# Kernel optimization log

Measured on AMD Instinct MI355X. Metric: run time of the kernel, lower is better.

## Reference

```python
import jax, jax.numpy as jnp
import numpy as np

B, T, E, H, DK, FF = 8, 2048, 64, 8, 8, 256
EPS = 1e-5


def _ln(x, g, b):
    m = jnp.mean(x, axis=-1, keepdims=True)
    v = jnp.mean((x - m) ** 2, axis=-1, keepdims=True)
    return (x - m) * jax.lax.rsqrt(v + EPS) * g + b


def setup_inputs() -> dict:
    key = jax.random.key(0)
    ks = jax.random.split(key, 16)
    s = 0.05
    f32 = jnp.float32
    return {
        "x": jax.random.normal(ks[0], (B, T, E), f32),
        "Wq": jax.random.normal(ks[1], (E, E), f32) * s,
        "bq": jnp.zeros((E,), f32),
        "Wk": jax.random.normal(ks[2], (E, E), f32) * s,
        "bk": jnp.zeros((E,), f32),
        "Wv": jax.random.normal(ks[3], (E, E), f32) * s,
        "bv": jnp.zeros((E,), f32),
        "Wo": jax.random.normal(ks[4], (E, E), f32) * s,
        "bo": jnp.zeros((E,), f32),
        "theta_attn": jax.random.uniform(ks[5], (), f32, 0.0, 2.0 * np.pi),
        "theta_ffn": jax.random.uniform(ks[6], (), f32, 0.0, 2.0 * np.pi),
        "W1": jax.random.normal(ks[7], (FF, E), f32) * s,
        "b1": jnp.zeros((FF,), f32),
        "W2": jax.random.normal(ks[8], (E, FF), f32) * s,
        "b2": jnp.zeros((E,), f32),
        "g1": jnp.ones((E,), f32),
        "be1": jnp.zeros((E,), f32),
        "g2": jnp.ones((E,), f32),
        "be2": jnp.zeros((E,), f32),
    }


def _forward(x, Wq, bq, Wk, bk, Wv, bv, Wo, bo, theta_attn, theta_ffn,
             W1, b1, W2, b2, g1, be1, g2, be2):
    def split(h):  # [B,T,E] -> [B,H,T,DK]
        return h.reshape(B, T, H, DK).transpose(0, 2, 1, 3)

    q = split(x @ Wq.T + bq)
    k = split(x @ Wk.T + bk)
    v = split(x @ Wv.T + bv)
    # per-head quantum circuit: RX(x) then shared RX(theta) -> <Z> = cos(x + theta)
    q = jnp.cos(q + theta_attn)
    k = jnp.cos(k + theta_attn)
    v = jnp.cos(v + theta_attn)
    scores = jnp.einsum('bhtd,bhsd->bhts', q, k) / np.float32(np.sqrt(DK))
    scores = jax.nn.softmax(scores, axis=-1)
    attn = jnp.einsum('bhts,bhsd->bhtd', scores, v)
    attn = attn.transpose(0, 2, 1, 3).reshape(B, T, E) @ Wo.T + bo
    x1 = _ln(x + attn, g1, be1)
    # FFN quantum circuit: RX(x) then shared RY(theta) -> <Z> = cos(x)*cos(theta)
    qout = jnp.cos(x1) * jnp.cos(theta_ffn)
    f = jax.nn.relu(qout @ W1.T + b1) @ W2.T + b2
    return _ln(x1 + f, g2, be2)


def reference(x, Wq, bq, Wk, bk, Wv, bv, Wo, bo, theta_attn, theta_ffn,
              W1, b1, W2, b2, g1, be1, g2, be2):
    return _forward(x, Wq, bq, Wk, bk, Wv, bv, Wo, bo, theta_attn, theta_ffn,
                    W1, b1, W2, b2, g1, be1, g2, be2)
```

## Files before the change

kernel.cpp:

```cpp
#include <hip/hip_runtime.h>
#include <hip/hip_bf16.h>

#define B_ 8
#define T_ 2048
#define NROWS 16384

typedef __attribute__((ext_vector_type(4))) float f32x4;
typedef __attribute__((ext_vector_type(16))) float f32x16;
typedef __attribute__((ext_vector_type(8))) short short8;
typedef __fp16 half2_t __attribute__((ext_vector_type(2)));

__device__ __forceinline__ unsigned short f2bf(float f) {
    __hip_bfloat16 h = __float2bfloat16(f);
    return *reinterpret_cast<unsigned short*>(&h);
}
__device__ __forceinline__ unsigned int pkrtz(float a, float b) {
    half2_t h = __builtin_amdgcn_cvt_pkrtz(a, b);
    return __builtin_bit_cast(unsigned int, h);
}
__device__ __forceinline__ float dot2(unsigned int a, unsigned int b, float c) {
    return __builtin_amdgcn_fdot2(__builtin_bit_cast(half2_t, a),
                                  __builtin_bit_cast(half2_t, b), c, false);
}
__device__ __forceinline__ float fast_exp2(float x) {
#if __has_builtin(__builtin_amdgcn_exp2f)
    return __builtin_amdgcn_exp2f(x);
#else
    return exp2f(x);
#endif
}

__global__ __launch_bounds__(512, 4) void qkv_kernel(
    const float* __restrict__ x,
    const float* __restrict__ Wq, const float* __restrict__ bq,
    const float* __restrict__ Wk, const float* __restrict__ bk,
    const float* __restrict__ Wv, const float* __restrict__ bv,
    const float* __restrict__ theta_attn,
    unsigned short* __restrict__ qb, unsigned short* __restrict__ kbuf,
    unsigned short* __restrict__ vbuf)
{
    __shared__ unsigned int xpk[32][34];
    __shared__ unsigned int wpk[32][196];
    __shared__ unsigned short outs[32][216];
    const int tid = threadIdx.x;
    const int n0 = blockIdx.x * 32;

    {
        float4 v = ((const float4*)(x + (size_t)n0 * 64))[tid];
        int r = tid >> 4, k0 = (tid & 15) * 4;
        xpk[(k0 >> 1) + 0][r] = pkrtz(v.x, v.y);
        xpk[(k0 >> 1) + 1][r] = pkrtz(v.z, v.w);
    }
    const float* Wm[3] = {Wq, Wk, Wv};
    #pragma unroll
    for (int t = 0; t < 6; t++) {
        int fi = tid + t * 512;
        int m = fi >> 10, j = (fi >> 4) & 63, k0 = (fi & 15) * 4;
        float4 v = ((const float4*)Wm[m])[fi & 1023];
        wpk[(k0 >> 1) + 0][m * 64 + j] = pkrtz(v.x, v.y);
        wpk[(k0 >> 1) + 1][m * 64 + j] = pkrtz(v.z, v.w);
    }
    __syncthreads();

    const int r = tid >> 4;
    const int c0 = (tid & 15) * 12;
    float acc[12] = {};
    #pragma unroll 8
    for (int kp = 0; kp < 32; kp++) {
        unsigned int a = xpk[kp][r];
        uint4 b0 = *(const uint4*)&wpk[kp][c0];
        uint4 b1 = *(const uint4*)&wpk[kp][c0 + 4];
        uint4 b2 = *(const uint4*)&wpk[kp][c0 + 8];
        unsigned int bb[12] = {b0.x, b0.y, b0.z, b0.w,
                               b1.x, b1.y, b1.z, b1.w,
                               b2.x, b2.y, b2.z, b2.w};
        #pragma unroll
        for (int j = 0; j < 12; j++) acc[j] = dot2(a, bb[j], acc[j]);
    }

    const float th = *theta_attn;
    const float QS = 0.51006980f;
    const float* biasp[3] = {bq, bk, bv};
    {
        float vals[12];
        #pragma unroll
        for (int j = 0; j < 12; j++) {
            int c = c0 + j;
            int m = c >> 6, cc = c & 63;
            float v = __cosf(acc[j] + biasp[m][cc] + th);
            vals[j] = (m == 0) ? v * QS : v;
        }
        unsigned int* orow = (unsigned int*)&outs[r][c0];
        #pragma unroll
        for (int jp = 0; jp < 6; jp++)
            orow[jp] = (unsigned int)f2bf(vals[2 * jp]) |
                       ((unsigned int)f2bf(vals[2 * jp + 1]) << 16);
    }
    __syncthreads();

    unsigned short* outp3[3] = {qb, kbuf, vbuf};
    #pragma unroll
    for (int t = 0; t < 2; t++) {
        int fi = tid + t * 512;
        if (fi < 768) {
            int m = fi >> 8, rest = fi & 255;
            int hI = rest >> 5, r2 = rest & 31;
            uint4 v = *(const uint4*)&outs[r2][m * 64 + hI * 8];
            int n = n0 + r2;
            unsigned short* dst = outp3[m] +
                ((size_t)((n >> 11) * 8 + hI) * 2048 + (n & 2047)) * 8;
            *(uint4*)dst = v;
        }
    }
}

__global__ __launch_bounds__(256, 4) void attn_kernel(
    const unsigned short* __restrict__ qb,
    const unsigned short* __restrict__ kbuf,
    const unsigned short* __restrict__ vbuf,
    float* __restrict__ attn)
{
    __shared__ unsigned short Ks[1024 * 8];
    __shared__ unsigned short Vt[8 * 1032];
    const int tid = threadIdx.x;
    const int head = blockIdx.x >> 4;
    const int qblk = blockIdx.x & 15;
    const size_t hoff = (size_t)head * T_ * 8;
    const int wave = tid >> 6, lane = tid & 63;
    const int col = lane & 31, h = lane >> 5;
    const int q0 = qblk * 128 + wave * 32;

    const short8 z8 = {0, 0, 0, 0, 0, 0, 0, 0};
    short8 bqf = z8;
    if (h == 0) bqf = *(const short8*)(qb + hoff + (size_t)(q0 + col) * 8);

    f32x16 oacc = {0.f,0.f,0.f,0.f,0.f,0.f,0.f,0.f,0.f,0.f,0.f,0.f,0.f,0.f,0.f,0.f};
    const f32x16 z16 = {0.f,0.f,0.f,0.f,0.f,0.f,0.f,0.f,0.f,0.f,0.f,0.f,0.f,0.f,0.f,0.f};
    float lsum = 0.f;

    for (int half = 0; half < 2; half++) {
        __syncthreads();
        {
            const uint4* kg = (const uint4*)(kbuf + hoff + (size_t)half * 1024 * 8);
            const uint4* vg = (const uint4*)(vbuf + hoff + (size_t)half * 1024 * 8);
            uint4* kl = (uint4*)Ks;
            #pragma unroll
            for (int it = 0; it < 4; it++) {
                int s = tid + it * 256;
                kl[s] = kg[s];
                union { uint4 u; unsigned short us[8]; } cv;
                cv.u = vg[s];
                #pragma unroll
                for (int d = 0; d < 8; d++) Vt[d * 1032 + s] = cv.us[d];
            }
        }
        __syncthreads();

        for (int s0 = 0; s0 < 1024; s0 += 32) {
            short8 ak = z8;
            if (h == 0) ak = *(const short8*)&Ks[(s0 + col) * 8];
            f32x16 S = __builtin_amdgcn_mfma_f32_32x32x16_bf16(ak, bqf, z16, 0, 0, 0);
            float p[16];
            #pragma unroll
            for (int rr = 0; rr < 16; rr++) {
                p[rr] = fast_exp2(S[rr]);
                lsum += p[rr];
            }
            #pragma unroll
            for (int g = 0; g < 2; g++) {
                const float* pp = p + g * 8;
                unsigned int q01 = __builtin_amdgcn_perm(__float_as_uint(pp[1]), __float_as_uint(pp[0]), 0x07060302u);
                unsigned int q23 = __builtin_amdgcn_perm(__float_as_uint(pp[3]), __float_as_uint(pp[2]), 0x07060302u);
                unsigned int q45 = __builtin_amdgcn_perm(__float_as_uint(pp[5]), __float_as_uint(pp[4]), 0x07060302u);
                unsigned int q67 = __builtin_amdgcn_perm(__float_as_uint(pp[7]), __float_as_uint(pp[6]), 0x07060302u);
                unsigned int x01 = (unsigned int)__shfl_xor((int)q01, 32);
                unsigned int x23 = (unsigned int)__shfl_xor((int)q23, 32);
                unsigned int x45 = (unsigned int)__shfl_xor((int)q45, 32);
                unsigned int x67 = (unsigned int)__shfl_xor((int)q67, 32);
                union { unsigned int u[4]; short8 s; } bp;
                bp.u[0] = h ? x45 : q01;
                bp.u[1] = h ? x67 : q23;
                bp.u[2] = h ? q45 : x01;
                bp.u[3] = h ? q67 : x23;
                short8 av = z8;
                if (col < 8) av = *(const short8*)&Vt[col * 1032 + s0 + g * 16 + 8 * h];
                oacc = __builtin_amdgcn_mfma_f32_32x32x16_bf16(av, bp.s, oacc, 0, 0, 0);
            }
        }
    }

    lsum += __shfl_xor(lsum, 32);
    const float inv = 1.0f / lsum;
    const int bI = head >> 3, hI = head & 7;
    const int q = q0 + col;
    #pragma unroll
    for (int rr = 0; rr < 4; rr++) {
        int d = 4 * h + rr;
        attn[((size_t)bI * 2048 + q) * 64 + hI * 8 + d] = oacc[rr] * inv;
    }
}

__global__ __launch_bounds__(512, 4) void tail_kernel(
    const float* __restrict__ attn, const float* __restrict__ x,
    const float* __restrict__ Wo, const float* __restrict__ bo,
    const float* __restrict__ g1, const float* __restrict__ be1,
    const float* __restrict__ theta_ffn,
    const float* __restrict__ W1, const float* __restrict__ b1,
    const float* __restrict__ W2, const float* __restrict__ b2,
    const float* __restrict__ g2, const float* __restrict__ be2,
    float* __restrict__ outp)
{
    __shared__ unsigned int Wbuf[10880];
    __shared__ unsigned int qpk[32 * 34];
    __shared__ unsigned int Upk[128 * 34];
    const int tid = threadIdx.x;
    const int n0 = blockIdx.x * 32;
    const int r0 = tid >> 4;
    const int c0 = (tid & 15) * 4;
    unsigned int* const W1p = Wbuf + 2176;
    unsigned int* const W2p = Wbuf + 2176;

    float4 atv = ((const float4*)(attn + (size_t)n0 * 64))[tid];
    float4 wo0 = ((const float4*)Wo)[tid];
    float4 wo1 = ((const float4*)Wo)[tid + 512];
    float4 xv  = *(const float4*)(x + (size_t)(n0 + r0) * 64 + c0);
    float4 w1r[8];
    #pragma unroll
    for (int t = 0; t < 8; t++) w1r[t] = ((const float4*)W1)[tid + t * 512];

    {
        int rr = tid >> 4, k0 = (tid & 15) * 4;
        Upk[((k0 >> 1) + 0) * 34 + rr] = pkrtz(atv.x, atv.y);
        Upk[((k0 >> 1) + 1) * 34 + rr] = pkrtz(atv.z, atv.w);
    }
    {
        int nn = tid >> 4, k0 = (tid & 15) * 4;
        Wbuf[((k0 >> 1) + 0) * 68 + nn] = pkrtz(wo0.x, wo0.y);
        Wbuf[((k0 >> 1) + 1) * 68 + nn] = pkrtz(wo0.z, wo0.w);
        int fi = tid + 512;
        nn = fi >> 4; k0 = (fi & 15) * 4;
        Wbuf[((k0 >> 1) + 0) * 68 + nn] = pkrtz(wo1.x, wo1.y);
        Wbuf[((k0 >> 1) + 1) * 68 + nn] = pkrtz(wo1.z, wo1.w);
    }
    __syncthreads();

    #pragma unroll
    for (int t = 0; t < 8; t++) {
        int fi = tid + t * 512;
        int f = fi >> 4, k0 = (fi & 15) * 4;
        W1p[((k0 >> 1) + 0) * 260 + f] = pkrtz(w1r[t].x, w1r[t].y);
        W1p[((k0 >> 1) + 1) * 260 + f] = pkrtz(w1r[t].z, w1r[t].w);
    }

    float acc1[4] = {};
    #pragma unroll 8
    for (int kp = 0; kp < 32; kp++) {
        unsigned int a = Upk[kp * 34 + r0];
        uint4 b = *(const uint4*)&Wbuf[kp * 68 + c0];
        acc1[0] = dot2(a, b.x, acc1[0]);
        acc1[1] = dot2(a, b.y, acc1[1]);
        acc1[2] = dot2(a, b.z, acc1[2]);
        acc1[3] = dot2(a, b.w, acc1[3]);
    }

    float x1v[4];
    {
        float4 bo4 = *(const float4*)&bo[c0];
        float4 g14 = *(const float4*)&g1[c0];
        float4 be14 = *(const float4*)&be1[c0];
        float cth = __cosf(*theta_ffn);
        float vv[4] = {xv.x + acc1[0] + bo4.x, xv.y + acc1[1] + bo4.y,
                       xv.z + acc1[2] + bo4.z, xv.w + acc1[3] + bo4.w};
        float s1 = vv[0] + vv[1] + vv[2] + vv[3];
        float s2 = vv[0]*vv[0] + vv[1]*vv[1] + vv[2]*vv[2] + vv[3]*vv[3];
        #pragma unroll
        for (int m = 1; m <= 8; m <<= 1) {
            s1 += __shfl_xor(s1, m, 16);
            s2 += __shfl_xor(s2, m, 16);
        }
        float mean = s1 * 0.015625f;
        float rstd = rsqrtf(s2 * 0.015625f - mean * mean + 1e-5f);
        float gg[4] = {g14.x, g14.y, g14.z, g14.w};
        float eb[4] = {be14.x, be14.y, be14.z, be14.w};
        float qv[4];
        #pragma unroll
        for (int j = 0; j < 4; j++) {
            x1v[j] = (vv[j] - mean) * rstd * gg[j] + eb[j];
            qv[j] = __cosf(x1v[j]) * cth;
        }
        qpk[((c0 >> 1) + 0) * 34 + r0] = pkrtz(qv[0], qv[1]);
        qpk[((c0 >> 1) + 1) * 34 + r0] = pkrtz(qv[2], qv[3]);
    }
    __syncthreads();

    float4 w2r[8];
    #pragma unroll
    for (int t = 0; t < 8; t++) w2r[t] = ((const float4*)W2)[tid + t * 512];

    const int r2 = (tid >> 5) * 2;
    const int f0 = (tid & 31) * 8;
    float acc2[2][8] = {};
    #pragma unroll 4
    for (int kp = 0; kp < 32; kp++) {
        unsigned int a0 = qpk[kp * 34 + r2];
        unsigned int a1 = qpk[kp * 34 + r2 + 1];
        uint4 b0 = *(const uint4*)&W1p[kp * 260 + f0];
        uint4 b1_ = *(const uint4*)&W1p[kp * 260 + f0 + 4];
        unsigned int bb[8] = {b0.x, b0.y, b0.z, b0.w, b1_.x, b1_.y, b1_.z, b1_.w};
        #pragma unroll
        for (int j = 0; j < 8; j++) {
            acc2[0][j] = dot2(a0, bb[j], acc2[0][j]);
            acc2[1][j] = dot2(a1, bb[j], acc2[1][j]);
        }
    }
    {
        float4 c1a = *(const float4*)&b1[f0];
        float4 c1b = *(const float4*)&b1[f0 + 4];
        float bb[8] = {c1a.x, c1a.y, c1a.z, c1a.w, c1b.x, c1b.y, c1b.z, c1b.w};
        #pragma unroll
        for (int i = 0; i < 2; i++) {
            float hv[8];
            #pragma unroll
            for (int j = 0; j < 8; j++) hv[j] = fmaxf(acc2[i][j] + bb[j], 0.f);
            #pragma unroll
            for (int jp = 0; jp < 4; jp++)
                Upk[(f0 / 2 + jp) * 34 + r2 + i] = pkrtz(hv[2 * jp], hv[2 * jp + 1]);
        }
    }
    __syncthreads();

    #pragma unroll
    for (int t = 0; t < 8; t++) {
        int fi = tid + t * 512;
        int e = fi >> 6, k0 = (fi & 63) * 4;
        W2p[((k0 >> 1) + 0) * 68 + e] = pkrtz(w2r[t].x, w2r[t].y);
        W2p[((k0 >> 1) + 1) * 68 + e] = pkrtz(w2r[t].z, w2r[t].w);
    }
    __syncthreads();

    float acc3[4] = {};
    #pragma unroll 8
    for (int fp = 0; fp < 128; fp++) {
        unsigned int a = Upk[fp * 34 + r0];
        uint4 b = *(const uint4*)&W2p[fp * 68 + c0];
        acc3[0] = dot2(a, b.x, acc3[0]);
        acc3[1] = dot2(a, b.y, acc3[1]);
        acc3[2] = dot2(a, b.z, acc3[2]);
        acc3[3] = dot2(a, b.w, acc3[3]);
    }

    {
        float4 b24 = *(const float4*)&b2[c0];
        float4 g24 = *(const float4*)&g2[c0];
        float4 be24 = *(const float4*)&be2[c0];
        float vv[4] = {x1v[0] + acc3[0] + b24.x, x1v[1] + acc3[1] + b24.y,
                       x1v[2] + acc3[2] + b24.z, x1v[3] + acc3[3] + b24.w};
        float s1 = vv[0] + vv[1] + vv[2] + vv[3];
        float s2 = vv[0]*vv[0] + vv[1]*vv[1] + vv[2]*vv[2] + vv[3]*vv[3];
        #pragma unroll
        for (int m = 1; m <= 8; m <<= 1) {
            s1 += __shfl_xor(s1, m, 16);
            s2 += __shfl_xor(s2, m, 16);
        }
        float mean = s1 * 0.015625f;
        float rstd = rsqrtf(s2 * 0.015625f - mean * mean + 1e-5f);
        float4 o;
        o.x = (vv[0] - mean) * rstd * g24.x + be24.x;
        o.y = (vv[1] - mean) * rstd * g24.y + be24.y;
        o.z = (vv[2] - mean) * rstd * g24.z + be24.z;
        o.w = (vv[3] - mean) * rstd * g24.w + be24.w;
        *(float4*)(outp + (size_t)(n0 + r0) * 64 + c0) = o;
    }
}

extern "C" void kernel_launch(void* const* d_in, const int* in_sizes, int n_in,
                              void* d_out, int out_size, void* d_ws, size_t ws_size,
                              hipStream_t stream)
{
    const float* x   = (const float*)d_in[0];
    const float* Wq  = (const float*)d_in[1];
    const float* bq  = (const float*)d_in[2];
    const float* Wk  = (const float*)d_in[3];
    const float* bk  = (const float*)d_in[4];
    const float* Wv  = (const float*)d_in[5];
    const float* bv  = (const float*)d_in[6];
    const float* Wo  = (const float*)d_in[7];
    const float* bo  = (const float*)d_in[8];
    const float* tha = (const float*)d_in[9];
    const float* thf = (const float*)d_in[10];
    const float* W1  = (const float*)d_in[11];
    const float* b1  = (const float*)d_in[12];
    const float* W2  = (const float*)d_in[13];
    const float* b2  = (const float*)d_in[14];
    const float* g1  = (const float*)d_in[15];
    const float* be1 = (const float*)d_in[16];
    const float* g2  = (const float*)d_in[17];
    const float* be2 = (const float*)d_in[18];

    char* wsb = (char*)d_ws;
    unsigned short* qbp = (unsigned short*)(wsb);
    unsigned short* kbp = (unsigned short*)(wsb + (2u << 20));
    unsigned short* vbp = (unsigned short*)(wsb + (4u << 20));
    float* attn = (float*)(wsb + (6u << 20));

    qkv_kernel<<<512, 512, 0, stream>>>(x, Wq, bq, Wk, bk, Wv, bv, tha, qbp, kbp, vbp);
    attn_kernel<<<1024, 256, 0, stream>>>(qbp, kbp, vbp, attn);
    tail_kernel<<<512, 512, 0, stream>>>(attn, x, Wo, bo, g1, be1, thf,
                                         W1, b1, W2, b2, g2, be2, (float*)d_out);
}
```

Baseline: 165.4 us.

## Retile QKV and tail kernels, drop shuffles in attention P·V path

```diff
diff --git a/kernel.cpp b/kernel.cpp
--- a/kernel.cpp
+++ b/kernel.cpp
@@ -10,13 +10,12 @@
 typedef __attribute__((ext_vector_type(8))) short short8;
 typedef __fp16 half2_t __attribute__((ext_vector_type(2)));
 
-__device__ __forceinline__ unsigned short f2bf(float f) {
-    __hip_bfloat16 h = __float2bfloat16(f);
-    return *reinterpret_cast<unsigned short*>(&h);
-}
 __device__ __forceinline__ unsigned int pkrtz(float a, float b) {
     half2_t h = __builtin_amdgcn_cvt_pkrtz(a, b);
     return __builtin_bit_cast(unsigned int, h);
+}
+__device__ __forceinline__ unsigned int pkbf(float a, float b) {
+    return __builtin_amdgcn_perm(__float_as_uint(b), __float_as_uint(a), 0x07060302u);
 }
 __device__ __forceinline__ float dot2(unsigned int a, unsigned int b, float c) {
     return __builtin_amdgcn_fdot2(__builtin_bit_cast(half2_t, a),
@@ -30,7 +29,7 @@
 #endif
 }
 
-__global__ __launch_bounds__(512, 4) void qkv_kernel(
+__global__ __launch_bounds__(512, 2) void qkv_kernel(
     const float* __restrict__ x,
     const float* __restrict__ Wq, const float* __restrict__ bq,
     const float* __restrict__ Wk, const float* __restrict__ bk,
@@ -39,17 +38,19 @@
     unsigned short* __restrict__ qb, unsigned short* __restrict__ kbuf,
     unsigned short* __restrict__ vbuf)
 {
-    __shared__ unsigned int xpk[32][34];
-    __shared__ unsigned int wpk[32][196];
-    __shared__ unsigned short outs[32][216];
+    __shared__ unsigned int xpk[32 * 66];
+    __shared__ unsigned int wpk[32 * 196];
+    __shared__ unsigned int outs[6144];
     const int tid = threadIdx.x;
-    const int n0 = blockIdx.x * 32;
-
-    {
-        float4 v = ((const float4*)(x + (size_t)n0 * 64))[tid];
-        int r = tid >> 4, k0 = (tid & 15) * 4;
-        xpk[(k0 >> 1) + 0][r] = pkrtz(v.x, v.y);
-        xpk[(k0 >> 1) + 1][r] = pkrtz(v.z, v.w);
+    const int n0 = blockIdx.x * 64;
+
+    #pragma unroll
+    for (int t = 0; t < 2; t++) {
+        int fi = tid + t * 512;
+        float4 v = ((const float4*)(x + (size_t)n0 * 64))[fi];
+        int r = fi >> 4, k0 = (fi & 15) * 4;
+        xpk[(k0 >> 1) * 66 + r] = pkrtz(v.x, v.y);
+        xpk[((k0 >> 1) + 1) * 66 + r] = pkrtz(v.z, v.w);
     }
     const float* Wm[3] = {Wq, Wk, Wv};
     #pragma unroll
@@ -57,60 +58,69 @@
         int fi = tid + t * 512;
         int m = fi >> 10, j = (fi >> 4) & 63, k0 = (fi & 15) * 4;
         float4 v = ((const float4*)Wm[m])[fi & 1023];
-        wpk[(k0 >> 1) + 0][m * 64 + j] = pkrtz(v.x, v.y);
-        wpk[(k0 >> 1) + 1][m * 64 + j] = pkrtz(v.z, v.w);
-    }
-    __syncthreads();
-
-    const int r = tid >> 4;
-    const int c0 = (tid & 15) * 12;
-    float acc[12] = {};
+        wpk[(k0 >> 1) * 196 + m * 64 + j] = pkrtz(v.x, v.y);
+        wpk[((k0 >> 1) + 1) * 196 + m * 64 + j] = pkrtz(v.z, v.w);
+    }
+    __syncthreads();
+
+    const int r0 = (tid & 31) * 2;
+    const int c0 = (tid >> 5) * 12;
+    float acc[2][12] = {};
     #pragma unroll 8
     for (int kp = 0; kp < 32; kp++) {
-        unsigned int a = xpk[kp][r];
-        uint4 b0 = *(const uint4*)&wpk[kp][c0];
-        uint4 b1 = *(const uint4*)&wpk[kp][c0 + 4];
-        uint4 b2 = *(const uint4*)&wpk[kp][c0 + 8];
+        uint2 a = *(const uint2*)&xpk[kp * 66 + r0];
+        uint4 b0 = *(const uint4*)&wpk[kp * 196 + c0];
+        uint4 b1 = *(const uint4*)&wpk[kp * 196 + c0 + 4];
+        uint4 b2 = *(const uint4*)&wpk[kp * 196 + c0 + 8];
         unsigned int bb[12] = {b0.x, b0.y, b0.z, b0.w,
                                b1.x, b1.y, b1.z, b1.w,
                                b2.x, b2.y, b2.z, b2.w};
         #pragma unroll
-        for (int j = 0; j < 12; j++) acc[j] = dot2(a, bb[j], acc[j]);
-    }
-
-    const float th = *theta_attn;
-    const float QS = 0.51006980f;
-    const float* biasp[3] = {bq, bk, bv};
+        for (int j = 0; j < 12; j++) {
+            acc[0][j] = dot2(a.x, bb[j], acc[0][j]);
+            acc[1][j] = dot2(a.y, bb[j], acc[1][j]);
+        }
+    }
+
     {
-        float vals[12];
+        const float th = *theta_attn;
+        const float QS = 0.51006980f;
+        const float* biasp[3] = {bq, bk, bv};
+        float bcol[12];
         #pragma unroll
         for (int j = 0; j < 12; j++) {
             int c = c0 + j;
-            int m = c >> 6, cc = c & 63;
-            float v = __cosf(acc[j] + biasp[m][cc] + th);
-            vals[j] = (m == 0) ? v * QS : v;
-        }
-        unsigned int* orow = (unsigned int*)&outs[r][c0];
-        #pragma unroll
-        for (int jp = 0; jp < 6; jp++)
-            orow[jp] = (unsigned int)f2bf(vals[2 * jp]) |
-                       ((unsigned int)f2bf(vals[2 * jp + 1]) << 16);
+            bcol[j] = biasp[c >> 6][c & 63];
+        }
+        #pragma unroll
+        for (int i = 0; i < 2; i++) {
+            float vals[12];
+            #pragma unroll
+            for (int j = 0; j < 12; j++) {
+                float v = __cosf(acc[i][j] + bcol[j] + th);
+                vals[j] = ((c0 + j) >> 6) == 0 ? v * QS : v;
+            }
+            int row = r0 + i;
+            #pragma unroll
+            for (int t = 0; t < 6; t++) {
+                int c = c0 + 2 * t;
+                outs[(c >> 3) * 256 + row * 4 + ((c & 7) >> 1)] = pkbf(vals[2*t], vals[2*t+1]);
+            }
+        }
     }
     __syncthreads();
 
     unsigned short* outp3[3] = {qb, kbuf, vbuf};
     #pragma unroll
-    for (int t = 0; t < 2; t++) {
+    for (int t = 0; t < 3; t++) {
         int fi = tid + t * 512;
-        if (fi < 768) {
-            int m = fi >> 8, rest = fi & 255;
-            int hI = rest >> 5, r2 = rest & 31;
-            uint4 v = *(const uint4*)&outs[r2][m * 64 + hI * 8];
-            int n = n0 + r2;
-            unsigned short* dst = outp3[m] +
-                ((size_t)((n >> 11) * 8 + hI) * 2048 + (n & 2047)) * 8;
-            *(uint4*)dst = v;
-        }
+        int bh = fi >> 6, r2 = fi & 63;
+        int m = bh >> 3, hI = bh & 7;
+        uint4 v = *(const uint4*)&outs[4 * fi];
+        int n = n0 + r2;
+        unsigned short* dst = outp3[m] +
+            ((size_t)((n >> 11) * 8 + hI) * 2048 + (n & 2047)) * 8;
+        *(uint4*)dst = v;
     }
 }
 
@@ -169,21 +179,19 @@
             #pragma unroll
             for (int g = 0; g < 2; g++) {
                 const float* pp = p + g * 8;
-                unsigned int q01 = __builtin_amdgcn_perm(__float_as_uint(pp[1]), __float_as_uint(pp[0]), 0x07060302u);
-                unsigned int q23 = __builtin_amdgcn_perm(__float_as_uint(pp[3]), __float_as_uint(pp[2]), 0x07060302u);
-                unsigned int q45 = __builtin_amdgcn_perm(__float_as_uint(pp[5]), __float_as_uint(pp[4]), 0x07060302u);
-                unsigned int q67 = __builtin_amdgcn_perm(__float_as_uint(pp[7]), __float_as_uint(pp[6]), 0x07060302u);
-                unsigned int x01 = (unsigned int)__shfl_xor((int)q01, 32);
-                unsigned int x23 = (unsigned int)__shfl_xor((int)q23, 32);
-                unsigned int x45 = (unsigned int)__shfl_xor((int)q45, 32);
-                unsigned int x67 = (unsigned int)__shfl_xor((int)q67, 32);
                 union { unsigned int u[4]; short8 s; } bp;
-                bp.u[0] = h ? x45 : q01;
-                bp.u[1] = h ? x67 : q23;
-                bp.u[2] = h ? q45 : x01;
-                bp.u[3] = h ? q67 : x23;
+                bp.u[0] = pkbf(pp[0], pp[1]);
+                bp.u[1] = pkbf(pp[2], pp[3]);
+                bp.u[2] = pkbf(pp[4], pp[5]);
+                bp.u[3] = pkbf(pp[6], pp[7]);
                 short8 av = z8;
-                if (col < 8) av = *(const short8*)&Vt[col * 1032 + s0 + g * 16 + 8 * h];
+                if (col < 8) {
+                    const unsigned short* vp = &Vt[col * 1032 + s0 + g * 16 + h * 4];
+                    union { uint2 u2[2]; short8 s; } va;
+                    va.u2[0] = *(const uint2*)(vp);
+                    va.u2[1] = *(const uint2*)(vp + 8);
+                    av = va.s;
+                }
                 oacc = __builtin_amdgcn_mfma_f32_32x32x16_bf16(av, bp.s, oacc, 0, 0, 0);
             }
         }
@@ -210,37 +218,39 @@
     const float* __restrict__ g2, const float* __restrict__ be2,
     float* __restrict__ outp)
 {
-    __shared__ unsigned int Wbuf[10880];
+    __shared__ unsigned int Wbuf[10496];
     __shared__ unsigned int qpk[32 * 34];
-    __shared__ unsigned int Upk[128 * 34];
+    __shared__ unsigned int Upk[32 * 132];
     const int tid = threadIdx.x;
+    const int lane = tid & 63;
     const int n0 = blockIdx.x * 32;
-    const int r0 = tid >> 4;
-    const int c0 = (tid & 15) * 4;
     unsigned int* const W1p = Wbuf + 2176;
-    unsigned int* const W2p = Wbuf + 2176;
+    unsigned int* const W2p = Wbuf;
+    unsigned int* const hrow = Upk;
+
+    const int rp = ((tid >> 6) & 3) * 4 + (lane & 3);
+    const int r0 = rp * 2;
+    const int c0 = ((lane >> 2) & 15) * 4;
 
     float4 atv = ((const float4*)(attn + (size_t)n0 * 64))[tid];
     float4 wo0 = ((const float4*)Wo)[tid];
     float4 wo1 = ((const float4*)Wo)[tid + 512];
-    float4 xv  = *(const float4*)(x + (size_t)(n0 + r0) * 64 + c0);
+    float4 xv0 = *(const float4*)(x + (size_t)(n0 + r0) * 64 + c0);
+    float4 xv1 = *(const float4*)(x + (size_t)(n0 + r0 + 1) * 64 + c0);
     float4 w1r[8];
     #pragma unroll
     for (int t = 0; t < 8; t++) w1r[t] = ((const float4*)W1)[tid + t * 512];
 
     {
-        int rr = tid >> 4, k0 = (tid & 15) * 4;
-        Upk[((k0 >> 1) + 0) * 34 + rr] = pkrtz(atv.x, atv.y);
-        Upk[((k0 >> 1) + 1) * 34 + rr] = pkrtz(atv.z, atv.w);
-    }
-    {
-        int nn = tid >> 4, k0 = (tid & 15) * 4;
-        Wbuf[((k0 >> 1) + 0) * 68 + nn] = pkrtz(wo0.x, wo0.y);
-        Wbuf[((k0 >> 1) + 1) * 68 + nn] = pkrtz(wo0.z, wo0.w);
+        int r = tid >> 4, k0 = (tid & 15) * 4;
+        Upk[(k0 >> 1) * 34 + r] = pkrtz(atv.x, atv.y);
+        Upk[((k0 >> 1) + 1) * 34 + r] = pkrtz(atv.z, atv.w);
+        Wbuf[(k0 >> 1) * 68 + r] = pkrtz(wo0.x, wo0.y);
+        Wbuf[((k0 >> 1) + 1) * 68 + r] = pkrtz(wo0.z, wo0.w);
         int fi = tid + 512;
-        nn = fi >> 4; k0 = (fi & 15) * 4;
-        Wbuf[((k0 >> 1) + 0) * 68 + nn] = pkrtz(wo1.x, wo1.y);
-        Wbuf[((k0 >> 1) + 1) * 68 + nn] = pkrtz(wo1.z, wo1.w);
+        int r2 = fi >> 4, k2 = (fi & 15) * 4;
+        Wbuf[(k2 >> 1) * 68 + r2] = pkrtz(wo1.x, wo1.y);
+        Wbuf[((k2 >> 1) + 1) * 68 + r2] = pkrtz(wo1.z, wo1.w);
     }
     __syncthreads();
 
@@ -248,48 +258,54 @@
     for (int t = 0; t < 8; t++) {
         int fi = tid + t * 512;
         int f = fi >> 4, k0 = (fi & 15) * 4;
-        W1p[((k0 >> 1) + 0) * 260 + f] = pkrtz(w1r[t].x, w1r[t].y);
+        W1p[(k0 >> 1) * 260 + f] = pkrtz(w1r[t].x, w1r[t].y);
         W1p[((k0 >> 1) + 1) * 260 + f] = pkrtz(w1r[t].z, w1r[t].w);
     }
 
-    float acc1[4] = {};
-    #pragma unroll 8
-    for (int kp = 0; kp < 32; kp++) {
-        unsigned int a = Upk[kp * 34 + r0];
-        uint4 b = *(const uint4*)&Wbuf[kp * 68 + c0];
-        acc1[0] = dot2(a, b.x, acc1[0]);
-        acc1[1] = dot2(a, b.y, acc1[1]);
-        acc1[2] = dot2(a, b.z, acc1[2]);
-        acc1[3] = dot2(a, b.w, acc1[3]);
-    }
-
-    float x1v[4];
-    {
+    float x1v[2][4];
+    if (tid < 256) {
+        float acc1[2][4] = {};
+        #pragma unroll 8
+        for (int kp = 0; kp < 32; kp++) {
+            uint2 a = *(const uint2*)&Upk[kp * 34 + r0];
+            uint4 b = *(const uint4*)&Wbuf[kp * 68 + c0];
+            unsigned int bb[4] = {b.x, b.y, b.z, b.w};
+            #pragma unroll
+            for (int j = 0; j < 4; j++) {
+                acc1[0][j] = dot2(a.x, bb[j], acc1[0][j]);
+                acc1[1][j] = dot2(a.y, bb[j], acc1[1][j]);
+            }
+        }
         float4 bo4 = *(const float4*)&bo[c0];
         float4 g14 = *(const float4*)&g1[c0];
         float4 be14 = *(const float4*)&be1[c0];
-        float cth = __cosf(*theta_ffn);
-        float vv[4] = {xv.x + acc1[0] + bo4.x, xv.y + acc1[1] + bo4.y,
-                       xv.z + acc1[2] + bo4.z, xv.w + acc1[3] + bo4.w};
-        float s1 = vv[0] + vv[1] + vv[2] + vv[3];
-        float s2 = vv[0]*vv[0] + vv[1]*vv[1] + vv[2]*vv[2] + vv[3]*vv[3];
-        #pragma unroll
-        for (int m = 1; m <= 8; m <<= 1) {
-            s1 += __shfl_xor(s1, m, 16);
-            s2 += __shfl_xor(s2, m, 16);
-        }
-        float mean = s1 * 0.015625f;
-        float rstd = rsqrtf(s2 * 0.015625f - mean * mean + 1e-5f);
         float gg[4] = {g14.x, g14.y, g14.z, g14.w};
         float eb[4] = {be14.x, be14.y, be14.z, be14.w};
-        float qv[4];
-        #pragma unroll
-        for (int j = 0; j < 4; j++) {
-            x1v[j] = (vv[j] - mean) * rstd * gg[j] + eb[j];
-            qv[j] = __cosf(x1v[j]) * cth;
-        }
-        qpk[((c0 >> 1) + 0) * 34 + r0] = pkrtz(qv[0], qv[1]);
-        qpk[((c0 >> 1) + 1) * 34 + r0] = pkrtz(qv[2], qv[3]);
+        float bb4[4] = {bo4.x, bo4.y, bo4.z, bo4.w};
+        float cth = __cosf(*theta_ffn);
+        #pragma unroll
+        for (int i = 0; i < 2; i++) {
+            float4 xv = i ? xv1 : xv0;
+            float vv[4] = {xv.x + acc1[i][0] + bb4[0], xv.y + acc1[i][1] + bb4[1],
+                           xv.z + acc1[i][2] + bb4[2], xv.w + acc1[i][3] + bb4[3]};
+            float s1 = vv[0] + vv[1] + vv[2] + vv[3];
+            float s2 = vv[0]*vv[0] + vv[1]*vv[1] + vv[2]*vv[2] + vv[3]*vv[3];
+            #pragma unroll
+            for (int m = 4; m <= 32; m <<= 1) {
+                s1 += __shfl_xor(s1, m);
+                s2 += __shfl_xor(s2, m);
+            }
+            float mean = s1 * 0.015625f;
+            float rstd = rsqrtf(s2 * 0.015625f - mean * mean + 1e-5f);
+            float qv[4];
+            #pragma unroll
+            for (int j = 0; j < 4; j++) {
+                x1v[i][j] = (vv[j] - mean) * rstd * gg[j] + eb[j];
+                qv[j] = __cosf(x1v[i][j]) * cth;
+            }
+            qpk[((c0 >> 1) + 0) * 34 + r0 + i] = pkrtz(qv[0], qv[1]);
+            qpk[((c0 >> 1) + 1) * 34 + r0 + i] = pkrtz(qv[2], qv[3]);
+        }
     }
     __syncthreads();
 
@@ -297,23 +313,22 @@
     #pragma unroll
     for (int t = 0; t < 8; t++) w2r[t] = ((const float4*)W2)[tid + t * 512];
 
-    const int r2 = (tid >> 5) * 2;
-    const int f0 = (tid & 31) * 8;
-    float acc2[2][8] = {};
-    #pragma unroll 4
-    for (int kp = 0; kp < 32; kp++) {
-        unsigned int a0 = qpk[kp * 34 + r2];
-        unsigned int a1 = qpk[kp * 34 + r2 + 1];
-        uint4 b0 = *(const uint4*)&W1p[kp * 260 + f0];
-        uint4 b1_ = *(const uint4*)&W1p[kp * 260 + f0 + 4];
-        unsigned int bb[8] = {b0.x, b0.y, b0.z, b0.w, b1_.x, b1_.y, b1_.z, b1_.w};
-        #pragma unroll
-        for (int j = 0; j < 8; j++) {
-            acc2[0][j] = dot2(a0, bb[j], acc2[0][j]);
-            acc2[1][j] = dot2(a1, bb[j], acc2[1][j]);
-        }
-    }
     {
+        const int r2 = (tid & 15) * 2;
+        const int f0 = (tid >> 4) * 8;
+        float acc2[2][8] = {};
+        #pragma unroll 4
+        for (int kp = 0; kp < 32; kp++) {
+            uint2 a = *(const uint2*)&qpk[kp * 34 + r2];
+            uint4 b0 = *(const uint4*)&W1p[kp * 260 + f0];
+            uint4 b1q = *(const uint4*)&W1p[kp * 260 + f0 + 4];
+            unsigned int bb[8] = {b0.x, b0.y, b0.z, b0.w, b1q.x, b1q.y, b1q.z, b1q.w};
+            #pragma unroll
+            for (int j = 0; j < 8; j++) {
+                acc2[0][j] = dot2(a.x, bb[j], acc2[0][j]);
+                acc2[1][j] = dot2(a.y, bb[j], acc2[1][j]);
+            }
+        }
         float4 c1a = *(const float4*)&b1[f0];
         float4 c1b = *(const float4*)&b1[f0 + 4];
         float bb[8] = {c1a.x, c1a.y, c1a.z, c1a.w, c1b.x, c1b.y, c1b.z, c1b.w};
@@ -322,9 +337,10 @@
             float hv[8];
             #pragma unroll
             for (int j = 0; j < 8; j++) hv[j] = fmaxf(acc2[i][j] + bb[j], 0.f);
-            #pragma unroll
-            for (int jp = 0; jp < 4; jp++)
-                Upk[(f0 / 2 + jp) * 34 + r2 + i] = pkrtz(hv[2 * jp], hv[2 * jp + 1]);
+            uint4 hq;
+            hq.x = pkrtz(hv[0], hv[1]); hq.y = pkrtz(hv[2], hv[3]);
+            hq.z = pkrtz(hv[4], hv[5]); hq.w = pkrtz(hv[6], hv[7]);
+            *(uint4*)&hrow[(r2 + i) * 132 + (f0 >> 1)] = hq;
         }
     }
     __syncthreads();
@@ -333,43 +349,62 @@
     for (int t = 0; t < 8; t++) {
         int fi = tid + t * 512;
         int e = fi >> 6, k0 = (fi & 63) * 4;
-        W2p[((k0 >> 1) + 0) * 68 + e] = pkrtz(w2r[t].x, w2r[t].y);
+        W2p[(k0 >> 1) * 68 + e] = pkrtz(w2r[t].x, w2r[t].y);
         W2p[((k0 >> 1) + 1) * 68 + e] = pkrtz(w2r[t].z, w2r[t].w);
     }
     __syncthreads();
 
-    float acc3[4] = {};
-    #pragma unroll 8
-    for (int fp = 0; fp < 128; fp++) {
-        unsigned int a = Upk[fp * 34 + r0];
-        uint4 b = *(const uint4*)&W2p[fp * 68 + c0];
-        acc3[0] = dot2(a, b.x, acc3[0]);
-        acc3[1] = dot2(a, b.y, acc3[1]);
-        acc3[2] = dot2(a, b.z, acc3[2]);
-        acc3[3] = dot2(a, b.w, acc3[3]);
-    }
-
-    {
+    if (tid < 256) {
+        float acc3[2][4] = {};
+        #pragma unroll 4
+        for (int fp0 = 0; fp0 < 128; fp0 += 4) {
+            uint4 a0 = *(const uint4*)&hrow[(r0 + 0) * 132 + fp0];
+            uint4 a1 = *(const uint4*)&hrow[(r0 + 1) * 132 + fp0];
+            uint4 b0 = *(const uint4*)&W2p[(fp0 + 0) * 68 + c0];
+            uint4 b1q = *(const uint4*)&W2p[(fp0 + 1) * 68 + c0];
+            uint4 b2q = *(const uint4*)&W2p[(fp0 + 2) * 68 + c0];
+            uint4 b3q = *(const uint4*)&W2p[(fp0 + 3) * 68 + c0];
+            unsigned int aa[2][4] = {{a0.x, a0.y, a0.z, a0.w},
+                                     {a1.x, a1.y, a1.z, a1.w}};
+            unsigned int bbb[4][4] = {{b0.x, b0.y, b0.z, b0.w},
+                                      {b1q.x, b1q.y, b1q.z, b1q.w},
+                                      {b2q.x, b2q.y, b2q.z, b2q.w},
+                                      {b3q.x, b3q.y, b3q.z, b3q.w}};
+            #pragma unroll
+            for (int i = 0; i < 2; i++)
+                #pragma unroll
+                for (int j = 0; j < 4; j++) {
+                    float t0 = dot2(aa[i][0], bbb[0][j], acc3[i][j]);
+                    t0 = dot2(aa[i][1], bbb[1][j], t0);
+                    t0 = dot2(aa[i][2], bbb[2][j], t0);
+                    acc3[i][j] = dot2(aa[i][3], bbb[3][j], t0);
+                }
+        }
         float4 b24 = *(const float4*)&b2[c0];
         float4 g24 = *(const float4*)&g2[c0];
         float4 be24 = *(const float4*)&be2[c0];
-        float vv[4] = {x1v[0] + acc3[0] + b24.x, x1v[1] + acc3[1] + b24.y,
-                       x1v[2] + acc3[2] + b24.z, x1v[3] + acc3[3] + b24.w};
-        float s1 = vv[0] + vv[1] + vv[2] + vv[3];
-        float s2 = vv[0]*vv[0] + vv[1]*vv[1] + vv[2]*vv[2] + vv[3]*vv[3];
-        #pragma unroll
-        for (int m = 1; m <= 8; m <<= 1) {
-            s1 += __shfl_xor(s1, m, 16);
-            s2 += __shfl_xor(s2, m, 16);
-        }
-        float mean = s1 * 0.015625f;
-        float rstd = rsqrtf(s2 * 0.015625f - mean * mean + 1e-5f);
-        float4 o;
-        o.x = (vv[0] - mean) * rstd * g24.x + be24.x;
-        o.y = (vv[1] - mean) * rstd * g24.y + be24.y;
-        o.z = (vv[2] - mean) * rstd * g24.z + be24.z;
-        o.w = (vv[3] - mean) * rstd * g24.w + be24.w;
-        *(float4*)(outp + (size_t)(n0 + r0) * 64 + c0) = o;
+        #pragma unroll
+        for (int i = 0; i < 2; i++) {
+            float vv[4] = {x1v[i][0] + acc3[i][0] + b24.x,
+                           x1v[i][1] + acc3[i][1] + b24.y,
+                           x1v[i][2] + acc3[i][2] + b24.z,
+                           x1v[i][3] + acc3[i][3] + b24.w};
+            float s1 = vv[0] + vv[1] + vv[2] + vv[3];
+            float s2 = vv[0]*vv[0] + vv[1]*vv[1] + vv[2]*vv[2] + vv[3]*vv[3];
+            #pragma unroll
+            for (int m = 4; m <= 32; m <<= 1) {
+                s1 += __shfl_xor(s1, m);
+                s2 += __shfl_xor(s2, m);
+            }
+            float mean = s1 * 0.015625f;
+            float rstd = rsqrtf(s2 * 0.015625f - mean * mean + 1e-5f);
+            float4 o;
+            o.x = (vv[0] - mean) * rstd * g24.x + be24.x;
+            o.y = (vv[1] - mean) * rstd * g24.y + be24.y;
+            o.z = (vv[2] - mean) * rstd * g24.z + be24.z;
+            o.w = (vv[3] - mean) * rstd * g24.w + be24.w;
+            *(float4*)(outp + (size_t)(n0 + r0 + i) * 64 + c0) = o;
+        }
     }
 }
 
@@ -403,7 +438,7 @@
     unsigned short* vbp = (unsigned short*)(wsb + (4u << 20));
     float* attn = (float*)(wsb + (6u << 20));
 
-    qkv_kernel<<<512, 512, 0, stream>>>(x, Wq, bq, Wk, bk, Wv, bv, tha, qbp, kbp, vbp);
+    qkv_kernel<<<256, 512, 0, stream>>>(x, Wq, bq, Wk, bk, Wv, bv, tha, qbp, kbp, vbp);
     attn_kernel<<<1024, 256, 0, stream>>>(qbp, kbp, vbp, attn);
     tail_kernel<<<512, 512, 0, stream>>>(attn, x, Wo, bo, g1, be1, thf,
                                          W1, b1, W2, b2, g2, be2, (float*)d_out);
```

Result: faster. 158.6 us (-4.1%).
